# Kernel tuning notes

Measured on AMD Instinct MI355X. Metric: run time of the kernel, lower is better.

## Reference

```python
import jax, jax.numpy as jnp
import numpy as np
from jax import lax

B, L, C, H, W = 16, 8, 64, 50, 50
OC, K, PAD = 64, 3, 1
CQ = C // 16


def conv2d(x, w, b, pad):
    y = lax.conv_general_dilated(x, w, (1, 1), [(pad, pad), (pad, pad)],
                                 dimension_numbers=('NCHW', 'OIHW', 'NCHW'))
    return y + b[None, :, None, None]


def attention(x, y, q_w, q_b, k_w, k_b, v_w, v_b):
    # x, y: [b, C, 5, 5]
    b, c, h, w = x.shape
    q = conv2d(x, q_w, q_b, 1).reshape(b, -1, h * w)   # [b, CQ, N]
    kk = conv2d(y, k_w, k_b, 1).reshape(b, -1, h * w)  # [b, CQ, N]
    attn = jax.nn.softmax(jnp.einsum('bcn,bcm->bnm', q, kk), axis=-1)  # [b, Nq, Nk]
    v = conv2d(y, v_w, v_b, 1).reshape(b, c, h * w)    # [b, C, N]
    out = jnp.einsum('bcm,bnm->bcn', v, attn)          # bmm(V, attn^T)
    return out.reshape(b, c, h, w)


def setup_inputs():
    key = jax.random.key(0)
    ks = jax.random.split(key, 15)
    s = 0.05
    return {
        'x': jax.random.normal(ks[0], (B, L, C, H, W), jnp.float32),
        'weight': jax.random.normal(ks[1], (OC, C, K, K), jnp.float32) * s,
        'bias': jax.random.normal(ks[2], (OC,), jnp.float32) * s,
        'init_w': jax.random.normal(ks[3], (C, C, 3, 3), jnp.float32) * s,
        'init_b': jax.random.normal(ks[4], (C,), jnp.float32) * s,
        'q_w': jax.random.normal(ks[5], (CQ, C, 3, 3), jnp.float32) * s,
        'q_b': jax.random.normal(ks[6], (CQ,), jnp.float32) * s,
        'k_w': jax.random.normal(ks[7], (CQ, C, 3, 3), jnp.float32) * s,
        'k_b': jax.random.normal(ks[8], (CQ,), jnp.float32) * s,
        'v_w': jax.random.normal(ks[9], (C, C, 3, 3), jnp.float32) * s,
        'v_b': jax.random.normal(ks[10], (C,), jnp.float32) * s,
        'tconv_w': jax.random.normal(ks[11], (C, C), jnp.float32) * s,  # 1x1x1 Conv3d C->C
        'tconv_b': jax.random.normal(ks[12], (C,), jnp.float32) * s,
        'fc_w': jax.random.normal(ks[13], (C,), jnp.float32) * s,       # 1x1x1 Conv3d C->1
        'fc_b': jax.random.normal(ks[14], (), jnp.float32) * s,
    }


def reference(x, weight, bias, init_w, init_b, q_w, q_b, k_w, k_b, v_w, v_b,
              tconv_w, tconv_b, fc_w, fc_b):
    b, l, c, h, w = x.shape
    # --- generateweight ---
    xet = jnp.transpose(x, (0, 2, 1, 3, 4))  # [b, c, l, h, w]
    # AdaptiveMaxPool3d((None,5,5)); h,w multiples of 5 -> exact reshape max
    pooled = xet.reshape(b, c, l, 5, h // 5, 5, w // 5).max((4, 6))  # [b,c,l,5,5]
    seq = jnp.moveaxis(pooled, 2, 0)  # [l, b, c, 5, 5]
    prior0 = conv2d(seq[0], init_w, init_b, 1)

    def step(prior, xt):
        new = attention(prior, xt, q_w, q_b, k_w, k_b, v_w, v_b)
        return new, new

    _, allp = lax.scan(step, prior0, seq)            # [l, b, c, 5, 5]
    avg = jnp.moveaxis(allp, 0, 2).mean((3, 4))      # AdaptiveAvgPool3d -> [b, c, l]
    calib = jnp.einsum('oc,bcl->bol', tconv_w, avg) + tconv_b[None, :, None]  # [b,c,l]
    scale = 1.0 + jnp.transpose(calib, (0, 2, 1))    # [b, l, c]
    # finalweight[b,l,o,i,kh,kw] = weight[o,i,kh,kw] * scale[b,l,i]
    fw = weight[None, None] * scale[:, :, None, :, None, None]
    fc_out = jnp.einsum('c,bcl->bl', fc_w, avg) + fc_b  # [b, l]
    fb = bias[None, None, :] * (1.0 + fc_out)[:, :, None]  # [b, l, oc]
    # --- grouped conv with groups = b*l ---
    xg = x.reshape(1, b * l * c, h, w)
    wg = fw.reshape(b * l * OC, c, K, K)
    out = lax.conv_general_dilated(xg, wg, (1, 1), [(PAD, PAD), (PAD, PAD)],
                                   feature_group_count=b * l,
                                   dimension_numbers=('NCHW', 'OIHW', 'NCHW'))
    out = out.reshape(b * l, OC, out.shape[-2], out.shape[-1])
    out = out + fb.reshape(b * l, OC)[:, :, None, None]
    return out
```

## Files before the change

kernel.cpp:

```cpp
#include <hip/hip_runtime.h>

typedef short s16x8 __attribute__((ext_vector_type(8)));
typedef float f32x4 __attribute__((ext_vector_type(4)));
typedef unsigned int u32x4 __attribute__((ext_vector_type(4)));

__device__ __forceinline__ unsigned short bf16r(float f) {
  unsigned int u = __float_as_uint(f);
  u += 0x7fffu + ((u >> 16) & 1u);
  return (unsigned short)(u >> 16);
}
__device__ __forceinline__ float bf_lo(unsigned int u) {
  return __uint_as_float(u << 16);
}
__device__ __forceinline__ float bf_hi(unsigned int u) {
  return __uint_as_float(u & 0xffff0000u);
}


__global__ __launch_bounds__(256) void poolprep2_kernel(
    const float* __restrict__ x, float* __restrict__ pooled,
    unsigned short* __restrict__ xs) {
  const int blk = blockIdx.x;
  const int g = blk / 10;
  const int rem = blk % 10;
  const int band = rem >> 1;
  const int chalf = rem & 1;
  const int ch0 = chalf * 4;
  const float* xg = x + (size_t)g * 160000;
  unsigned short* xsg = xs + (size_t)g * (52 * 52 * 64);
  __shared__ float pm2[32 * 250];
  const int tid = threadIdx.x;

  for (int task = tid; task < 1000; task += 256) {
    int chunk4 = task & 3;
    int rest = task >> 2;
    int xpair = rest % 25;
    int r = rest / 25;
    int y = band * 10 + r;
    int chunk = ch0 + chunk4;
    const float* base = xg + (chunk * 8) * 2500 + y * 50 + xpair * 2;
    float2 v[8];
#pragma unroll
    for (int k = 0; k < 8; ++k) v[k] = *(const float2*)(base + k * 2500);
#pragma unroll
    for (int k = 0; k < 8; ++k)
      pm2[(chunk4 * 8 + k) * 250 + r * 25 + xpair] = fmaxf(v[k].x, v[k].y);
    uint4 a, b;
    a.x = (unsigned)bf16r(v[0].x) | ((unsigned)bf16r(v[1].x) << 16);
    a.y = (unsigned)bf16r(v[2].x) | ((unsigned)bf16r(v[3].x) << 16);
    a.z = (unsigned)bf16r(v[4].x) | ((unsigned)bf16r(v[5].x) << 16);
    a.w = (unsigned)bf16r(v[6].x) | ((unsigned)bf16r(v[7].x) << 16);
    b.x = (unsigned)bf16r(v[0].y) | ((unsigned)bf16r(v[1].y) << 16);
    b.y = (unsigned)bf16r(v[2].y) | ((unsigned)bf16r(v[3].y) << 16);
    b.z = (unsigned)bf16r(v[4].y) | ((unsigned)bf16r(v[5].y) << 16);
    b.w = (unsigned)bf16r(v[6].y) | ((unsigned)bf16r(v[7].y) << 16);
    int xx = xpair * 2;
    *(uint4*)&xsg[(((y + 1) * 52) + (xx + 1)) * 64 + chunk * 8] = a;
    *(uint4*)&xsg[(((y + 1) * 52) + (xx + 2)) * 64 + chunk * 8] = b;
  }
  uint4 z4;
  z4.x = 0; z4.y = 0; z4.z = 0; z4.w = 0;
  for (int task = tid; task < 80; task += 256) {
    int chunk4 = task & 3;
    int rest = task >> 2;
    int col = (rest & 1) ? 51 : 0;
    int r = rest >> 1;
    int y = band * 10 + r;
    *(uint4*)&xsg[(((y + 1) * 52) + col) * 64 + (ch0 + chunk4) * 8] = z4;
  }
  if (band == 0) {
    for (int task = tid; task < 208; task += 256)
      *(uint4*)&xsg[(task >> 2) * 64 + (ch0 + (task & 3)) * 8] = z4;
  }
  if (band == 4) {
    for (int task = tid; task < 208; task += 256)
      *(uint4*)&xsg[(51 * 52 + (task >> 2)) * 64 + (ch0 + (task & 3)) * 8] = z4;
  }
  __syncthreads();
  if (tid < 160) {
    int c_local = tid / 5, ox = tid % 5;
    const float* pr = &pm2[c_local * 250 + ox * 5];
    float m = -1e30f;
#pragma unroll
    for (int r = 0; r < 10; ++r) {
#pragma unroll
      for (int xp = 0; xp < 5; ++xp) m = fmaxf(m, pr[r * 25 + xp]);
    }
    int c_g = chalf * 32 + c_local;
    pooled[(size_t)g * 1600 + c_g * 25 + band * 5 + ox] = m;
  }
}

__device__ __forceinline__ void conv_pass2(
    const unsigned short* in_s, const unsigned short* __restrict__ wg,
    f32x4 acc[4][4], int ikk, int wave, int lane, int l15, int l4) {
#pragma unroll
  for (int dy = 0; dy < 3; ++dy) {
    const int rr = wave + dy;
#pragma unroll
    for (int dx = 0; dx < 3; ++dx) {
      const int tap = dy * 3 + dx;
      s16x8 a[4], bfr[4];
#pragma unroll
      for (int mf = 0; mf < 4; ++mf)
        a[mf] = *reinterpret_cast<const s16x8*>(
            wg + ((((tap * 2 + ikk) * 4 + mf) * 64 + lane) << 3));
#pragma unroll
      for (int nf = 0; nf < 4; ++nf) {
        int cc = nf * 16 + l15 + dx;
        int slot = l4 ^ ((cc >> 1) & 3);
        bfr[nf] = *reinterpret_cast<const s16x8*>(
            &in_s[((rr * 66 + cc) << 5) + (slot << 3)]);
      }
#pragma unroll
      for (int mf = 0; mf < 4; ++mf)
#pragma unroll
        for (int nf = 0; nf < 4; ++nf)
          acc[mf][nf] = __builtin_amdgcn_mfma_f32_16x16x32_bf16(
              a[mf], bfr[nf], acc[mf][nf], 0, 0, 0);
    }
  }
}

__global__ __launch_bounds__(512, 4) void conv_main_fast4(
    const unsigned short* __restrict__ xs, const unsigned short* __restrict__ wt3,
    const float* __restrict__ fb_g, float* __restrict__ out) {
  const int g = blockIdx.x & 127;
  const int band = blockIdx.x >> 7;
  const int y0 = band * 8;
  const int tid = threadIdx.x;
  __shared__ __align__(16) unsigned short in_s[10 * 66 * 32];
  __shared__ float fb_s[64];
  if (tid < 64) fb_s[tid] = fb_g[g * 64 + tid];

  const unsigned short* xsg = xs + (size_t)g * (52 * 52 * 64);
  const unsigned short* wg = wt3 + (size_t)g * 36864;
  const int wave = tid >> 6, lane = tid & 63;
  const int l15 = lane & 15, l4 = lane >> 4;
  const int yrow = y0 + wave;

  f32x4 acc[4][4];
  f32x4 z = {0.f, 0.f, 0.f, 0.f};
#pragma unroll
  for (int mf = 0; mf < 4; ++mf)
#pragma unroll
    for (int nf = 0; nf < 4; ++nf) acc[mf][nf] = z;

  for (int task = tid; task < 2640; task += 512) {
    int slot = task & 3;
    int c = (task >> 2) % 66;
    int r = (task >> 2) / 66;
    int py = y0 + r;
    int srcSub = slot ^ ((c >> 1) & 3);
    const unsigned short* src = xsg + ((size_t)(py * 52 + c) * 64 + srcSub * 8);
    unsigned short* ldsb = in_s + (size_t)(task & ~63) * 8;
    __builtin_amdgcn_global_load_lds(
        (const __attribute__((address_space(1))) void*)src,
        (__attribute__((address_space(3))) void*)ldsb, 16, 0, 0);
  }
  __syncthreads();
  if (yrow < 50) conv_pass2(in_s, wg, acc, 0, wave, lane, l15, l4);
  __syncthreads();
  for (int task = tid; task < 2640; task += 512) {
    int slot = task & 3;
    int c = (task >> 2) % 66;
    int r = (task >> 2) / 66;
    int py = y0 + r;
    int srcSub = slot ^ ((c >> 1) & 3);
    const unsigned short* src = xsg + ((size_t)(py * 52 + c) * 64 + 32 + srcSub * 8);
    unsigned short* ldsb = in_s + (size_t)(task & ~63) * 8;
    __builtin_amdgcn_global_load_lds(
        (const __attribute__((address_space(1))) void*)src,
        (__attribute__((address_space(3))) void*)ldsb, 16, 0, 0);
  }
  __syncthreads();
  if (yrow < 50) {
    conv_pass2(in_s, wg, acc, 1, wave, lane, l15, l4);
    float* og = out + (size_t)g * 64 * 2500 + yrow * 50;
#pragma unroll
    for (int mf = 0; mf < 4; ++mf) {
#pragma unroll
      for (int r = 0; r < 4; ++r) {
        int o = mf * 16 + l4 * 4 + r;
        float fbv = fb_s[o];
#pragma unroll
        for (int nf = 0; nf < 4; ++nf) {
          int xx = nf * 16 + l15;
          if (xx < 50) og[(size_t)o * 2500 + xx] = acc[mf][nf][r] + fbv;
        }
      }
    }
  }
}

__global__ __launch_bounds__(256) void calwt_kernel(
    const float* __restrict__ avgg, const float* __restrict__ tconvw,
    const float* __restrict__ tconvb, const float* __restrict__ fcw,
    const float* __restrict__ fcb, const float* __restrict__ bias,
    const float* __restrict__ w, float* __restrict__ fb_g,
    unsigned short* __restrict__ wt3) {
  const int g = blockIdx.x;
  const int tid = threadIdx.x;
  __shared__ float tcw_s[64 * 65];
  __shared__ float av[64];
  __shared__ float sc[64];
  for (int idx = tid; idx < 4096; idx += 256)
    tcw_s[(idx >> 6) * 65 + (idx & 63)] = tconvw[idx];
  if (tid < 64) av[tid] = avgg[g * 64 + tid];
  __syncthreads();
  if (tid < 64) {
    int o = tid;
    float cal = tconvb[o];
#pragma unroll
    for (int c = 0; c < 64; ++c) cal += tcw_s[o * 65 + c] * av[c];
    sc[o] = 1.0f + cal;
    float part = fcw[o] * av[o];
#pragma unroll
    for (int off = 32; off; off >>= 1) part += __shfl_down(part, off);
    float fc = __shfl(part, 0) + fcb[0];
    fb_g[g * 64 + o] = bias[o] * (1.0f + fc);
  }
  __syncthreads();
  unsigned short* outg = wt3 + (size_t)g * 36864;
  for (int idx = tid; idx < 36864; idx += 256) {
    int j = idx & 7;
    int lane = (idx >> 3) & 63;
    int mf = (idx >> 9) & 3;
    int ik = (idx >> 11) & 1;
    int tap = idx >> 12;
    int o = mf * 16 + (lane & 15);
    int i = ik * 32 + 8 * (lane >> 4) + j;
    outg[idx] = bf16r(w[((o * 64) + i) * 9 + tap] * sc[i]);
  }
}


__device__ __forceinline__ void conv64core(const float* pool_s,
                                           const float* __restrict__ wgt,
                                           float* red, int tid) {
  int co = tid & 63, qd = tid >> 6;
  float acc[25];
#pragma unroll
  for (int n = 0; n < 25; ++n) acc[n] = 0.f;
  for (int ci = qd * 16; ci < qd * 16 + 16; ++ci) {
    float in[25];
#pragma unroll
    for (int n = 0; n < 25; ++n) in[n] = pool_s[ci * 25 + n];
    float w9[9];
#pragma unroll
    for (int tp = 0; tp < 9; ++tp) w9[tp] = wgt[(co * 64 + ci) * 9 + tp];
#pragma unroll
    for (int n = 0; n < 25; ++n) {
      int y = n / 5, xx = n % 5;
#pragma unroll
      for (int dy = 0; dy < 3; ++dy) {
        int yy = y + dy - 1;
        if (yy < 0 || yy > 4) continue;
#pragma unroll
        for (int dx = 0; dx < 3; ++dx) {
          int xc = xx + dx - 1;
          if (xc < 0 || xc > 4) continue;
          acc[n] += in[yy * 5 + xc] * w9[dy * 3 + dx];
        }
      }
    }
  }
#pragma unroll
  for (int n = 0; n < 25; ++n) red[(qd * 64 + co) * 25 + n] = acc[n];
  __syncthreads();
}

__global__ __launch_bounds__(256) void convB2_kernel(
    const float* __restrict__ pooled, const float* __restrict__ vw,
    const float* __restrict__ vb, const float* __restrict__ kw,
    const float* __restrict__ kb, const float* __restrict__ iw,
    const float* __restrict__ ib, unsigned short* __restrict__ vbg,
    float* __restrict__ kk4g, float* __restrict__ p28g) {
  const int blk = blockIdx.x;
  __shared__ float pool_s[1600];
  __shared__ float red[6400];
  const int tid = threadIdx.x;
  for (int idx = tid; idx < 1600; idx += 256) pool_s[idx] = pooled[blk * 1600 + idx];
  __syncthreads();

  conv64core(pool_s, vw, red, tid);
  {
    unsigned short* dst = vbg + (size_t)blk * 2560;
    for (int idx = tid; idx < 1600; idx += 256) {
      float s = red[idx] + red[1600 + idx] + red[3200 + idx] + red[4800 + idx];
      dst[(idx / 25) * 40 + idx % 25] = bf16r(s + vb[idx / 25]);
    }
    for (int idx = tid; idx < 960; idx += 256)
      dst[(idx / 15) * 40 + 25 + idx % 15] = 0;
  }
  __syncthreads();

  {
    int co = tid & 3, ci = tid >> 2;
    float acc[25];
#pragma unroll
    for (int n = 0; n < 25; ++n) acc[n] = 0.f;
    float in[25];
#pragma unroll
    for (int n = 0; n < 25; ++n) in[n] = pool_s[ci * 25 + n];
    float w9[9];
#pragma unroll
    for (int tp = 0; tp < 9; ++tp) w9[tp] = kw[(co * 64 + ci) * 9 + tp];
#pragma unroll
    for (int n = 0; n < 25; ++n) {
      int y = n / 5, xx = n % 5;
#pragma unroll
      for (int dy = 0; dy < 3; ++dy) {
        int yy = y + dy - 1;
        if (yy < 0 || yy > 4) continue;
#pragma unroll
        for (int dx = 0; dx < 3; ++dx) {
          int xc = xx + dx - 1;
          if (xc < 0 || xc > 4) continue;
          acc[n] += in[yy * 5 + xc] * w9[dy * 3 + dx];
        }
      }
    }
#pragma unroll
    for (int n = 0; n < 25; ++n) red[(ci * 4 + co) * 25 + n] = acc[n];
  }
  __syncthreads();
  if (tid < 100) {
    int co = tid / 25, m = tid % 25;
    float s = 0.f;
    for (int c = 0; c < 64; ++c) s += red[(c * 4 + co) * 25 + m];
    kk4g[blk * 100 + m * 4 + co] = s + kb[co];
  }
  __syncthreads();

  if ((blk & 7) == 0) {
    conv64core(pool_s, iw, red, tid);
    float* dst = p28g + (size_t)(blk >> 3) * 1792;
    for (int idx = tid; idx < 1600; idx += 256) {
      float s = red[idx] + red[1600 + idx] + red[3200 + idx] + red[4800 + idx];
      dst[(idx / 25) * 28 + idx % 25] = s + ib[idx / 25];
    }
  }
}


__global__ __launch_bounds__(256) void scan3_kernel(
    const unsigned short* __restrict__ vbg, const float* __restrict__ kk4g,
    const float* __restrict__ p28g, const float* __restrict__ qw,
    const float* __restrict__ qb, float* __restrict__ avgg) {
  const int b = blockIdx.x;
  const int tid = threadIdx.x;
  __shared__ __align__(16) unsigned short v_bf[8 * 64 * 40];
  __shared__ __align__(16) unsigned short attn_bf[25 * 32];
  __shared__ float p_s[64 * 28];
  __shared__ float red[100 * 68];
  __shared__ f32x4 kk4_s[8 * 25];
  __shared__ float q_s[100];
  __shared__ float qw_s[2304];
  __shared__ float avgp[256];
  __shared__ float qb_s[4];

  {
    const u32x4* vs = (const u32x4*)(vbg + (size_t)b * 20480);
    u32x4* vd = (u32x4*)v_bf;
    for (int i = tid; i < 2560; i += 256) vd[i] = vs[i];
    const f32x4* ks = (const f32x4*)(kk4g + b * 800);
    for (int i = tid; i < 200; i += 256) kk4_s[i] = ks[i];
    const f32x4* ps = (const f32x4*)(p28g + (size_t)b * 1792);
    f32x4* pd = (f32x4*)p_s;
    for (int i = tid; i < 448; i += 256) pd[i] = ps[i];
    const f32x4* qs = (const f32x4*)qw;
    f32x4* qd = (f32x4*)qw_s;
    for (int i = tid; i < 576; i += 256) qd[i] = qs[i];
    if (tid < 4) qb_s[tid] = qb[tid];
  }
  __syncthreads();

  const int qco = tid & 3, qci = tid >> 2;
  float qwr[9];
#pragma unroll
  for (int tp = 0; tp < 9; ++tp) qwr[tp] = qw_s[(qco * 64 + qci) * 9 + tp];

#pragma unroll 1
  for (int l = 0; l < 8; ++l) {
    {
      f32x4 i4[7];
      const f32x4* pr = (const f32x4*)&p_s[qci * 28];
#pragma unroll
      for (int j = 0; j < 7; ++j) i4[j] = pr[j];
      float in[25];
#pragma unroll
      for (int n = 0; n < 25; ++n) in[n] = i4[n >> 2][n & 3];
      float acc[25];
#pragma unroll
      for (int n = 0; n < 25; ++n) acc[n] = 0.f;
#pragma unroll
      for (int n = 0; n < 25; ++n) {
        int y = n / 5, xx = n % 5;
#pragma unroll
        for (int dy = 0; dy < 3; ++dy) {
          int yy = y + dy - 1;
          if (yy < 0 || yy > 4) continue;
#pragma unroll
          for (int dx = 0; dx < 3; ++dx) {
            int xc = xx + dx - 1;
            if (xc < 0 || xc > 4) continue;
            acc[n] += in[yy * 5 + xc] * qwr[dy * 3 + dx];
          }
        }
      }
#pragma unroll
      for (int n = 0; n < 25; ++n) red[(qco * 25 + n) * 68 + qci] = acc[n];
    }
    if (l > 0 && tid < 64) {
      f32x4 a4 = *(const f32x4*)&avgp[tid * 4];
      avgg[(b * 8 + l - 1) * 64 + tid] = (a4[0] + a4[1] + a4[2] + a4[3]) * 0.04f;
    }
    __syncthreads();

    if (tid < 200) {
      int row = tid >> 1, h = tid & 1;
      const f32x4* rp = (const f32x4*)&red[row * 68 + h * 32];
      float s = 0.f;
#pragma unroll
      for (int j = 0; j < 8; ++j) {
        f32x4 r4 = rp[j];
        s += r4[0] + r4[1] + r4[2] + r4[3];
      }
      s += __shfl_down(s, 1);
      if (h == 0) q_s[row] = s + qb_s[row / 25];
    }
    __syncthreads();

    if (tid < 25) {
      const int n = tid;
      const f32x4* kk = &kk4_s[l * 25];
      float q0 = q_s[n], q1 = q_s[25 + n], q2 = q_s[50 + n], q3 = q_s[75 + n];
      float row[25];
      float mx = -1e30f;
#pragma unroll
      for (int m = 0; m < 25; ++m) {
        f32x4 k4 = kk[m];
        float s = q0 * k4[0] + q1 * k4[1] + q2 * k4[2] + q3 * k4[3];
        row[m] = s;
        mx = fmaxf(mx, s);
      }
      float sm = 0.f;
#pragma unroll
      for (int m = 0; m < 25; ++m) {
        float e = __expf(row[m] - mx);
        row[m] = e;
        sm += e;
      }
      float inv = 1.0f / sm;
      unsigned int w16[16];
#pragma unroll
      for (int j = 0; j < 16; ++j) {
        float lo = (2 * j < 25) ? row[2 * j] * inv : 0.f;
        float hi = (2 * j + 1 < 25) ? row[2 * j + 1] * inv : 0.f;
        w16[j] = (unsigned)bf16r(lo) | ((unsigned)bf16r(hi) << 16);
      }
      u32x4* ad = (u32x4*)&attn_bf[n * 32];
      u32x4 d0 = {w16[0], w16[1], w16[2], w16[3]};
      u32x4 d1 = {w16[4], w16[5], w16[6], w16[7]};
      u32x4 d2 = {w16[8], w16[9], w16[10], w16[11]};
      u32x4 d3 = {w16[12], w16[13], w16[14], w16[15]};
      ad[0] = d0; ad[1] = d1; ad[2] = d2; ad[3] = d3;
    }
    __syncthreads();

    {
      const int c = tid & 63, grp = tid >> 6;
      const u32x4* vr = (const u32x4*)&v_bf[(l * 64 + c) * 40];
      u32x4 vv[4];
#pragma unroll
      for (int j = 0; j < 4; ++j) vv[j] = vr[j];
      float vf[25];
#pragma unroll
      for (int m = 0; m < 25; ++m) {
        unsigned int u = vv[m >> 3][(m >> 1) & 3];
        vf[m] = (m & 1) ? bf_hi(u) : bf_lo(u);
      }
      float partial = 0.f;
      for (int n = grp; n < 25; n += 4) {
        const u32x4* ar = (const u32x4*)&attn_bf[n * 32];
        u32x4 aa[4];
#pragma unroll
        for (int j = 0; j < 4; ++j) aa[j] = ar[j];
        float acc = 0.f;
#pragma unroll
        for (int m = 0; m < 25; ++m) {
          unsigned int u = aa[m >> 3][(m >> 1) & 3];
          float a = (m & 1) ? bf_hi(u) : bf_lo(u);
          acc += vf[m] * a;
        }
        p_s[c * 28 + n] = acc;
        partial += acc;
      }
      avgp[(c << 2) + grp] = partial;
    }
    __syncthreads();
  }
  if (tid < 64) {
    f32x4 a4 = *(const f32x4*)&avgp[tid * 4];
    avgg[(b * 8 + 7) * 64 + tid] = (a4[0] + a4[1] + a4[2] + a4[3]) * 0.04f;
  }
}


__global__ __launch_bounds__(256) void pool_kernel(const float* __restrict__ x,
                                                   float* __restrict__ pooled) {
  const int blk = blockIdx.x;
  const float* plane = x + (size_t)blk * 2500;
  __shared__ float pmax[250];
  const int t = threadIdx.x;
  if (t < 250) {
    int r = t / 5, cc = t % 5;
    const float* row = plane + r * 50 + cc * 10;
    float m = row[0];
#pragma unroll
    for (int j = 1; j < 10; ++j) m = fmaxf(m, row[j]);
    pmax[r * 5 + cc] = m;
  }
  __syncthreads();
  if (t < 25) {
    int pr = t / 5, cc = t % 5;
    float m = pmax[(pr * 10) * 5 + cc];
#pragma unroll
    for (int rr = 1; rr < 10; ++rr) m = fmaxf(m, pmax[(pr * 10 + rr) * 5 + cc]);
    pooled[(size_t)blk * 25 + t] = m;
  }
}

__global__ __launch_bounds__(256) void wt_kernel(const float* __restrict__ w,
                                                 unsigned short* __restrict__ wt2) {
  int idx = blockIdx.x * 256 + threadIdx.x;
  if (idx >= 36864) return;
  int j = idx & 7;
  int lane = (idx >> 3) & 63;
  int mf = (idx >> 9) & 3;
  int ik = (idx >> 11) & 1;
  int tap = idx >> 12;
  int o = mf * 16 + (lane & 15);
  int i = ik * 32 + 8 * (lane >> 4) + j;
  wt2[idx] = bf16r(w[((o * 64) + i) * 9 + tap]);
}

__global__ __launch_bounds__(256) void conv_main(
    const float* __restrict__ x, const unsigned short* __restrict__ wt2,
    const float* __restrict__ scale_g, const float* __restrict__ fb_g,
    float* __restrict__ out) {
  const int g = blockIdx.x & 127;
  const int band = blockIdx.x >> 7;
  const int y0 = band * 4;
  const int tid = threadIdx.x;
  __shared__ unsigned short in_s[6 * 66 * 64];
  __shared__ float scale_s[64], fb_s[64];
  if (tid < 64) {
    scale_s[tid] = scale_g[g * 64 + tid];
    fb_s[tid] = fb_g[g * 64 + tid];
  }
  __syncthreads();
  const float* xg = x + (size_t)g * 160000;
  for (int task = tid; task < 3168; task += 256) {
    int c = task % 66;
    int rc = task / 66;
    int r = rc >> 3;
    int chunk = rc & 7;
    int y = y0 - 1 + r;
    int xi = c - 1;
    unsigned int p0 = 0, p1 = 0, p2 = 0, p3 = 0;
    if (y >= 0 && y < 50 && xi >= 0 && xi < 50) {
      const float* px = xg + chunk * 8 * 2500 + y * 50 + xi;
      float f0 = px[0] * scale_s[chunk * 8 + 0];
      float f1 = px[2500] * scale_s[chunk * 8 + 1];
      float f2 = px[5000] * scale_s[chunk * 8 + 2];
      float f3 = px[7500] * scale_s[chunk * 8 + 3];
      float f4 = px[10000] * scale_s[chunk * 8 + 4];
      float f5 = px[12500] * scale_s[chunk * 8 + 5];
      float f6 = px[15000] * scale_s[chunk * 8 + 6];
      float f7 = px[17500] * scale_s[chunk * 8 + 7];
      p0 = (unsigned)bf16r(f0) | ((unsigned)bf16r(f1) << 16);
      p1 = (unsigned)bf16r(f2) | ((unsigned)bf16r(f3) << 16);
      p2 = (unsigned)bf16r(f4) | ((unsigned)bf16r(f5) << 16);
      p3 = (unsigned)bf16r(f6) | ((unsigned)bf16r(f7) << 16);
    }
    int chS = chunk ^ (c & 7);
    uint4* dst = (uint4*)&in_s[((r * 66 + c) << 6) + (chS << 3)];
    uint4 u4;
    u4.x = p0; u4.y = p1; u4.z = p2; u4.w = p3;
    *dst = u4;
  }
  __syncthreads();
  const int wave = tid >> 6, lane = tid & 63;
  const int l15 = lane & 15, l4 = lane >> 4;
  const int yrow = y0 + wave;
  if (yrow < 50) {
    f32x4 acc[4][4];
    f32x4 z = {0.f, 0.f, 0.f, 0.f};
#pragma unroll
    for (int mf = 0; mf < 4; ++mf)
#pragma unroll
      for (int nf = 0; nf < 4; ++nf) acc[mf][nf] = z;
#pragma unroll
    for (int dy = 0; dy < 3; ++dy) {
      const int rr = wave + dy;
#pragma unroll
      for (int dx = 0; dx < 3; ++dx) {
        const int tap = dy * 3 + dx;
#pragma unroll
        for (int ik = 0; ik < 2; ++ik) {
          s16x8 a[4], bfr[4];
#pragma unroll
          for (int mf = 0; mf < 4; ++mf)
            a[mf] = *reinterpret_cast<const s16x8*>(
                wt2 + ((((tap * 2 + ik) * 4 + mf) * 64 + lane) << 3));
#pragma unroll
          for (int nf = 0; nf < 4; ++nf) {
            int cc = nf * 16 + l15 + dx;
            int chS = (ik * 4 + l4) ^ (cc & 7);
            bfr[nf] = *reinterpret_cast<const s16x8*>(
                &in_s[((rr * 66 + cc) << 6) + (chS << 3)]);
          }
#pragma unroll
          for (int mf = 0; mf < 4; ++mf)
#pragma unroll
            for (int nf = 0; nf < 4; ++nf)
              acc[mf][nf] = __builtin_amdgcn_mfma_f32_16x16x32_bf16(
                  a[mf], bfr[nf], acc[mf][nf], 0, 0, 0);
        }
      }
    }
    float* og = out + (size_t)g * 64 * 2500 + yrow * 50;
#pragma unroll
    for (int mf = 0; mf < 4; ++mf) {
#pragma unroll
      for (int r = 0; r < 4; ++r) {
        int o = mf * 16 + l4 * 4 + r;
        float fbv = fb_s[o];
#pragma unroll
        for (int nf = 0; nf < 4; ++nf) {
          int xx = nf * 16 + l15;
          if (xx < 50) og[(size_t)o * 2500 + xx] = acc[mf][nf][r] + fbv;
        }
      }
    }
  }
}

__global__ __launch_bounds__(256) void calib_kernel(
    const float* __restrict__ avgg, const float* __restrict__ tconvw,
    const float* __restrict__ tconvb, const float* __restrict__ fcw,
    const float* __restrict__ fcb, const float* __restrict__ bias,
    float* __restrict__ scale_g, float* __restrict__ fb_g) {
  const int tid = threadIdx.x;
  const int wave = tid >> 6, o = tid & 63;
  const int bl = blockIdx.x * 4 + wave;
  __shared__ float tcw_s[64 * 65];
  __shared__ float avgl[4][64];
  for (int idx = tid; idx < 4096; idx += 256)
    tcw_s[(idx >> 6) * 65 + (idx & 63)] = tconvw[idx];
  avgl[wave][o] = avgg[bl * 64 + o];
  __syncthreads();
  float cal = tconvb[o];
  const float* av = avgl[wave];
#pragma unroll
  for (int c = 0; c < 64; ++c) cal += tcw_s[o * 65 + c] * av[c];
  scale_g[bl * 64 + o] = 1.0f + cal;
  float part = fcw[o] * av[o];
#pragma unroll
  for (int off = 32; off; off >>= 1) part += __shfl_down(part, off);
  float fc = __shfl(part, 0) + fcb[0];
  fb_g[bl * 64 + o] = bias[o] * (1.0f + fc);
}

extern "C" void kernel_launch(void* const* d_in, const int* in_sizes, int n_in,
                              void* d_out, int out_size, void* d_ws, size_t ws_size,
                              hipStream_t stream) {
  const float* x       = (const float*)d_in[0];
  const float* weight  = (const float*)d_in[1];
  const float* bias    = (const float*)d_in[2];
  const float* init_w  = (const float*)d_in[3];
  const float* init_b  = (const float*)d_in[4];
  const float* q_w     = (const float*)d_in[5];
  const float* q_b     = (const float*)d_in[6];
  const float* k_w     = (const float*)d_in[7];
  const float* k_b     = (const float*)d_in[8];
  const float* v_w     = (const float*)d_in[9];
  const float* v_b     = (const float*)d_in[10];
  const float* tconv_w = (const float*)d_in[11];
  const float* tconv_b = (const float*)d_in[12];
  const float* fc_w    = (const float*)d_in[13];
  const float* fc_b    = (const float*)d_in[14];
  float* out = (float*)d_out;

  float* ws = (float*)d_ws;
  float* pooled = ws;
  unsigned short* vbg = (unsigned short*)(ws + 204800);
  float* kk4g   = ws + 368640;
  float* p28g   = ws + 381440;
  float* scaleg = ws + 410112;
  float* fbg    = ws + 418304;
  float* avgg   = ws + 426496;
  unsigned short* wt3 = (unsigned short*)(ws + 434688);
  unsigned short* xsb = wt3 + 4718592;

  const size_t NEED_FAST = 55543808ull;

  if (ws_size >= NEED_FAST) {
    poolprep2_kernel<<<1280, 256, 0, stream>>>(x, pooled, xsb);
    convB2_kernel<<<128, 256, 0, stream>>>(pooled, v_w, v_b, k_w, k_b, init_w,
                                           init_b, vbg, kk4g, p28g);
    scan3_kernel<<<16, 256, 0, stream>>>(vbg, kk4g, p28g, q_w, q_b, avgg);
    calwt_kernel<<<128, 256, 0, stream>>>(avgg, tconv_w, tconv_b, fc_w, fc_b, bias,
                                          weight, fbg, wt3);
    conv_main_fast4<<<896, 512, 0, stream>>>(xsb, wt3, fbg, out);
  } else {
    unsigned short* wt2 = (unsigned short*)(ws + 434688);
    pool_kernel<<<8192, 256, 0, stream>>>(x, pooled);
    wt_kernel<<<144, 256, 0, stream>>>(weight, wt2);
    convB2_kernel<<<128, 256, 0, stream>>>(pooled, v_w, v_b, k_w, k_b, init_w,
                                           init_b, vbg, kk4g, p28g);
    scan3_kernel<<<16, 256, 0, stream>>>(vbg, kk4g, p28g, q_w, q_b, avgg);
    calib_kernel<<<32, 256, 0, stream>>>(avgg, tconv_w, tconv_b, fc_w, fc_b, bias,
                                         scaleg, fbg);
    conv_main<<<13 * 128, 256, 0, stream>>>(x, wt2, scaleg, fbg, out);
  }
}
```

Measured before the change: 151.5 us.

## Overlap bf16 input repacking with serial scan and double-buffer conv channel halves

Splits the pooling+repack kernel so the padded bf16 input repack runs as extra blocks inside the 16-block serial attention scan kernel. The repack then fills otherwise idle CUs while the scan runs, and the pool kernel gets lighter. The main conv now uses 6-row bands with 384 threads and separate LDS buffers for the two channel halves. This lets the second half's global-to-LDS load be issued before the first half's MFMA pass, removing one barrier. The cost is more blocks, more halo row reloads from the smaller bands, larger LDS per block, and dynamic shared memory for the scan kernel.

```diff
diff --git a/kernel.cpp b/kernel.cpp
--- a/kernel.cpp
+++ b/kernel.cpp
@@ -17,9 +17,8 @@
 }
 
 
-__global__ __launch_bounds__(256) void poolprep2_kernel(
-    const float* __restrict__ x, float* __restrict__ pooled,
-    unsigned short* __restrict__ xs) {
+__global__ __launch_bounds__(256) void pool3_kernel(
+    const float* __restrict__ x, float* __restrict__ pooled) {
   const int blk = blockIdx.x;
   const int g = blk / 10;
   const int rem = blk % 10;
@@ -27,7 +26,6 @@
   const int chalf = rem & 1;
   const int ch0 = chalf * 4;
   const float* xg = x + (size_t)g * 160000;
-  unsigned short* xsg = xs + (size_t)g * (52 * 52 * 64);
   __shared__ float pm2[32 * 250];
   const int tid = threadIdx.x;
 
@@ -45,6 +43,44 @@
 #pragma unroll
     for (int k = 0; k < 8; ++k)
       pm2[(chunk4 * 8 + k) * 250 + r * 25 + xpair] = fmaxf(v[k].x, v[k].y);
+  }
+  __syncthreads();
+  if (tid < 160) {
+    int c_local = tid / 5, ox = tid % 5;
+    const float* pr = &pm2[c_local * 250 + ox * 5];
+    float m = -1e30f;
+#pragma unroll
+    for (int r = 0; r < 10; ++r) {
+#pragma unroll
+      for (int xp = 0; xp < 5; ++xp) m = fmaxf(m, pr[r * 25 + xp]);
+    }
+    int c_g = chalf * 32 + c_local;
+    pooled[(size_t)g * 1600 + c_g * 25 + band * 5 + ox] = m;
+  }
+}
+
+__device__ __forceinline__ void xsprep_block(int blk, const float* __restrict__ x,
+                                             unsigned short* __restrict__ xs) {
+  const int g = blk / 10;
+  const int rem = blk % 10;
+  const int band = rem >> 1;
+  const int chalf = rem & 1;
+  const int ch0 = chalf * 4;
+  const float* xg = x + (size_t)g * 160000;
+  unsigned short* xsg = xs + (size_t)g * (52 * 52 * 64);
+  const int tid = threadIdx.x;
+
+  for (int task = tid; task < 1000; task += 256) {
+    int chunk4 = task & 3;
+    int rest = task >> 2;
+    int xpair = rest % 25;
+    int r = rest / 25;
+    int y = band * 10 + r;
+    int chunk = ch0 + chunk4;
+    const float* base = xg + (chunk * 8) * 2500 + y * 50 + xpair * 2;
+    float2 v[8];
+#pragma unroll
+    for (int k = 0; k < 8; ++k) v[k] = *(const float2*)(base + k * 2500);
     uint4 a, b;
     a.x = (unsigned)bf16r(v[0].x) | ((unsigned)bf16r(v[1].x) << 16);
     a.y = (unsigned)bf16r(v[2].x) | ((unsigned)bf16r(v[3].x) << 16);
@@ -76,18 +112,175 @@
     for (int task = tid; task < 208; task += 256)
       *(uint4*)&xsg[(51 * 52 + (task >> 2)) * 64 + (ch0 + (task & 3)) * 8] = z4;
   }
-  __syncthreads();
-  if (tid < 160) {
-    int c_local = tid / 5, ox = tid % 5;
-    const float* pr = &pm2[c_local * 250 + ox * 5];
-    float m = -1e30f;
-#pragma unroll
-    for (int r = 0; r < 10; ++r) {
-#pragma unroll
-      for (int xp = 0; xp < 5; ++xp) m = fmaxf(m, pr[r * 25 + xp]);
-    }
-    int c_g = chalf * 32 + c_local;
-    pooled[(size_t)g * 1600 + c_g * 25 + band * 5 + ox] = m;
+}
+
+__global__ __launch_bounds__(256) void scanx_kernel(
+    const unsigned short* __restrict__ vbg, const float* __restrict__ kk4g,
+    const float* __restrict__ p28g, const float* __restrict__ qw,
+    const float* __restrict__ qb, float* __restrict__ avgg,
+    const float* __restrict__ x, unsigned short* __restrict__ xs) {
+  if (blockIdx.x >= 16) {
+    xsprep_block(blockIdx.x - 16, x, xs);
+    return;
+  }
+  extern __shared__ __align__(16) char smem_raw[];
+  unsigned short* v_bf = (unsigned short*)smem_raw;
+  unsigned short* attn_bf = (unsigned short*)(smem_raw + 40960);
+  float* p_s = (float*)(smem_raw + 42560);
+  float* red = (float*)(smem_raw + 49728);
+  f32x4* kk4_s = (f32x4*)(smem_raw + 76928);
+  float* q_s = (float*)(smem_raw + 80128);
+  float* qw_s = (float*)(smem_raw + 80528);
+  float* avgp = (float*)(smem_raw + 89744);
+  float* qb_s = (float*)(smem_raw + 90768);
+
+  const int b = blockIdx.x;
+  const int tid = threadIdx.x;
+
+  {
+    const u32x4* vs = (const u32x4*)(vbg + (size_t)b * 20480);
+    u32x4* vd = (u32x4*)v_bf;
+    for (int i = tid; i < 2560; i += 256) vd[i] = vs[i];
+    const f32x4* ks = (const f32x4*)(kk4g + b * 800);
+    for (int i = tid; i < 200; i += 256) kk4_s[i] = ks[i];
+    const f32x4* ps = (const f32x4*)(p28g + (size_t)b * 1792);
+    f32x4* pd = (f32x4*)p_s;
+    for (int i = tid; i < 448; i += 256) pd[i] = ps[i];
+    const f32x4* qs = (const f32x4*)qw;
+    f32x4* qd = (f32x4*)qw_s;
+    for (int i = tid; i < 576; i += 256) qd[i] = qs[i];
+    if (tid < 4) qb_s[tid] = qb[tid];
+  }
+  __syncthreads();
+
+  const int qco = tid & 3, qci = tid >> 2;
+  float qwr[9];
+#pragma unroll
+  for (int tp = 0; tp < 9; ++tp) qwr[tp] = qw_s[(qco * 64 + qci) * 9 + tp];
+
+#pragma unroll 1
+  for (int l = 0; l < 8; ++l) {
+    {
+      f32x4 i4[7];
+      const f32x4* pr = (const f32x4*)&p_s[qci * 28];
+#pragma unroll
+      for (int j = 0; j < 7; ++j) i4[j] = pr[j];
+      float in[25];
+#pragma unroll
+      for (int n = 0; n < 25; ++n) in[n] = i4[n >> 2][n & 3];
+      float acc[25];
+#pragma unroll
+      for (int n = 0; n < 25; ++n) acc[n] = 0.f;
+#pragma unroll
+      for (int n = 0; n < 25; ++n) {
+        int y = n / 5, xx = n % 5;
+#pragma unroll
+        for (int dy = 0; dy < 3; ++dy) {
+          int yy = y + dy - 1;
+          if (yy < 0 || yy > 4) continue;
+#pragma unroll
+          for (int dx = 0; dx < 3; ++dx) {
+            int xc = xx + dx - 1;
+            if (xc < 0 || xc > 4) continue;
+            acc[n] += in[yy * 5 + xc] * qwr[dy * 3 + dx];
+          }
+        }
+      }
+#pragma unroll
+      for (int n = 0; n < 25; ++n) red[(qco * 25 + n) * 68 + qci] = acc[n];
+    }
+    if (l > 0 && tid < 64) {
+      f32x4 a4 = *(const f32x4*)&avgp[tid * 4];
+      avgg[(b * 8 + l - 1) * 64 + tid] = (a4[0] + a4[1] + a4[2] + a4[3]) * 0.04f;
+    }
+    __syncthreads();
+
+    if (tid < 200) {
+      int row = tid >> 1, h = tid & 1;
+      const f32x4* rp = (const f32x4*)&red[row * 68 + h * 32];
+      float s = 0.f;
+#pragma unroll
+      for (int j = 0; j < 8; ++j) {
+        f32x4 r4 = rp[j];
+        s += r4[0] + r4[1] + r4[2] + r4[3];
+      }
+      s += __shfl_down(s, 1);
+      if (h == 0) q_s[row] = s + qb_s[row / 25];
+    }
+    __syncthreads();
+
+    if (tid < 25) {
+      const int n = tid;
+      const f32x4* kk = &kk4_s[l * 25];
+      float q0 = q_s[n], q1 = q_s[25 + n], q2 = q_s[50 + n], q3 = q_s[75 + n];
+      float row[25];
+      float mx = -1e30f;
+#pragma unroll
+      for (int m = 0; m < 25; ++m) {
+        f32x4 k4 = kk[m];
+        float s = q0 * k4[0] + q1 * k4[1] + q2 * k4[2] + q3 * k4[3];
+        row[m] = s;
+        mx = fmaxf(mx, s);
+      }
+      float sm = 0.f;
+#pragma unroll
+      for (int m = 0; m < 25; ++m) {
+        float e = __expf(row[m] - mx);
+        row[m] = e;
+        sm += e;
+      }
+      float inv = 1.0f / sm;
+      unsigned int w16[16];
+#pragma unroll
+      for (int j = 0; j < 16; ++j) {
+        float lo = (2 * j < 25) ? row[2 * j] * inv : 0.f;
+        float hi = (2 * j + 1 < 25) ? row[2 * j + 1] * inv : 0.f;
+        w16[j] = (unsigned)bf16r(lo) | ((unsigned)bf16r(hi) << 16);
+      }
+      u32x4* ad = (u32x4*)&attn_bf[n * 32];
+      u32x4 d0 = {w16[0], w16[1], w16[2], w16[3]};
+      u32x4 d1 = {w16[4], w16[5], w16[6], w16[7]};
+      u32x4 d2 = {w16[8], w16[9], w16[10], w16[11]};
+      u32x4 d3 = {w16[12], w16[13], w16[14], w16[15]};
+      ad[0] = d0; ad[1] = d1; ad[2] = d2; ad[3] = d3;
+    }
+    __syncthreads();
+
+    {
+      const int c = tid & 63, grp = tid >> 6;
+      const u32x4* vr = (const u32x4*)&v_bf[(l * 64 + c) * 40];
+      u32x4 vv[4];
+#pragma unroll
+      for (int j = 0; j < 4; ++j) vv[j] = vr[j];
+      float vf[25];
+#pragma unroll
+      for (int m = 0; m < 25; ++m) {
+        unsigned int u = vv[m >> 3][(m >> 1) & 3];
+        vf[m] = (m & 1) ? bf_hi(u) : bf_lo(u);
+      }
+      float partial = 0.f;
+      for (int n = grp; n < 25; n += 4) {
+        const u32x4* ar = (const u32x4*)&attn_bf[n * 32];
+        u32x4 aa[4];
+#pragma unroll
+        for (int j = 0; j < 4; ++j) aa[j] = ar[j];
+        float acc = 0.f;
+#pragma unroll
+        for (int m = 0; m < 25; ++m) {
+          unsigned int u = aa[m >> 3][(m >> 1) & 3];
+          float a = (m & 1) ? bf_hi(u) : bf_lo(u);
+          acc += vf[m] * a;
+        }
+        p_s[c * 28 + n] = acc;
+        partial += acc;
+      }
+      avgp[(c << 2) + grp] = partial;
+    }
+    __syncthreads();
+  }
+  if (tid < 64) {
+    f32x4 a4 = *(const f32x4*)&avgp[tid * 4];
+    avgg[(b * 8 + 7) * 64 + tid] = (a4[0] + a4[1] + a4[2] + a4[3]) * 0.04f;
   }
 }
 
@@ -122,14 +315,15 @@
   }
 }
 
-__global__ __launch_bounds__(512, 4) void conv_main_fast4(
+__global__ __launch_bounds__(384, 3) void conv_main_fast5(
     const unsigned short* __restrict__ xs, const unsigned short* __restrict__ wt3,
     const float* __restrict__ fb_g, float* __restrict__ out) {
   const int g = blockIdx.x & 127;
   const int band = blockIdx.x >> 7;
-  const int y0 = band * 8;
+  const int y0 = band * 6;
   const int tid = threadIdx.x;
-  __shared__ __align__(16) unsigned short in_s[10 * 66 * 32];
+  __shared__ __align__(16) unsigned short in0[8 * 66 * 32];
+  __shared__ __align__(16) unsigned short in1[8 * 66 * 32];
   __shared__ float fb_s[64];
   if (tid < 64) fb_s[tid] = fb_g[g * 64 + tid];
 
@@ -146,36 +340,35 @@
 #pragma unroll
     for (int nf = 0; nf < 4; ++nf) acc[mf][nf] = z;
 
-  for (int task = tid; task < 2640; task += 512) {
+  for (int task = tid; task < 2112; task += 384) {
     int slot = task & 3;
     int c = (task >> 2) % 66;
     int r = (task >> 2) / 66;
     int py = y0 + r;
     int srcSub = slot ^ ((c >> 1) & 3);
     const unsigned short* src = xsg + ((size_t)(py * 52 + c) * 64 + srcSub * 8);
-    unsigned short* ldsb = in_s + (size_t)(task & ~63) * 8;
+    unsigned short* ldsb = in0 + (size_t)(task & ~63) * 8;
     __builtin_amdgcn_global_load_lds(
         (const __attribute__((address_space(1))) void*)src,
         (__attribute__((address_space(3))) void*)ldsb, 16, 0, 0);
   }
   __syncthreads();
-  if (yrow < 50) conv_pass2(in_s, wg, acc, 0, wave, lane, l15, l4);
-  __syncthreads();
-  for (int task = tid; task < 2640; task += 512) {
+  for (int task = tid; task < 2112; task += 384) {
     int slot = task & 3;
     int c = (task >> 2) % 66;
     int r = (task >> 2) / 66;
     int py = y0 + r;
     int srcSub = slot ^ ((c >> 1) & 3);
     const unsigned short* src = xsg + ((size_t)(py * 52 + c) * 64 + 32 + srcSub * 8);
-    unsigned short* ldsb = in_s + (size_t)(task & ~63) * 8;
+    unsigned short* ldsb = in1 + (size_t)(task & ~63) * 8;
     __builtin_amdgcn_global_load_lds(
         (const __attribute__((address_space(1))) void*)src,
         (__attribute__((address_space(3))) void*)ldsb, 16, 0, 0);
   }
+  if (yrow < 50) conv_pass2(in0, wg, acc, 0, wave, lane, l15, l4);
   __syncthreads();
   if (yrow < 50) {
-    conv_pass2(in_s, wg, acc, 1, wave, lane, l15, l4);
+    conv_pass2(in1, wg, acc, 1, wave, lane, l15, l4);
     float* og = out + (size_t)g * 64 * 2500 + yrow * 50;
 #pragma unroll
     for (int mf = 0; mf < 4; ++mf) {
@@ -340,170 +533,6 @@
       float s = red[idx] + red[1600 + idx] + red[3200 + idx] + red[4800 + idx];
       dst[(idx / 25) * 28 + idx % 25] = s + ib[idx / 25];
     }
-  }
-}
-
-
-__global__ __launch_bounds__(256) void scan3_kernel(
-    const unsigned short* __restrict__ vbg, const float* __restrict__ kk4g,
-    const float* __restrict__ p28g, const float* __restrict__ qw,
-    const float* __restrict__ qb, float* __restrict__ avgg) {
-  const int b = blockIdx.x;
-  const int tid = threadIdx.x;
-  __shared__ __align__(16) unsigned short v_bf[8 * 64 * 40];
-  __shared__ __align__(16) unsigned short attn_bf[25 * 32];
-  __shared__ float p_s[64 * 28];
-  __shared__ float red[100 * 68];
-  __shared__ f32x4 kk4_s[8 * 25];
-  __shared__ float q_s[100];
-  __shared__ float qw_s[2304];
-  __shared__ float avgp[256];
-  __shared__ float qb_s[4];
-
-  {
-    const u32x4* vs = (const u32x4*)(vbg + (size_t)b * 20480);
-    u32x4* vd = (u32x4*)v_bf;
-    for (int i = tid; i < 2560; i += 256) vd[i] = vs[i];
-    const f32x4* ks = (const f32x4*)(kk4g + b * 800);
-    for (int i = tid; i < 200; i += 256) kk4_s[i] = ks[i];
-    const f32x4* ps = (const f32x4*)(p28g + (size_t)b * 1792);
-    f32x4* pd = (f32x4*)p_s;
-    for (int i = tid; i < 448; i += 256) pd[i] = ps[i];
-    const f32x4* qs = (const f32x4*)qw;
-    f32x4* qd = (f32x4*)qw_s;
-    for (int i = tid; i < 576; i += 256) qd[i] = qs[i];
-    if (tid < 4) qb_s[tid] = qb[tid];
-  }
-  __syncthreads();
-
-  const int qco = tid & 3, qci = tid >> 2;
-  float qwr[9];
-#pragma unroll
-  for (int tp = 0; tp < 9; ++tp) qwr[tp] = qw_s[(qco * 64 + qci) * 9 + tp];
-
-#pragma unroll 1
-  for (int l = 0; l < 8; ++l) {
-    {
-      f32x4 i4[7];
-      const f32x4* pr = (const f32x4*)&p_s[qci * 28];
-#pragma unroll
-      for (int j = 0; j < 7; ++j) i4[j] = pr[j];
-      float in[25];
-#pragma unroll
-      for (int n = 0; n < 25; ++n) in[n] = i4[n >> 2][n & 3];
-      float acc[25];
-#pragma unroll
-      for (int n = 0; n < 25; ++n) acc[n] = 0.f;
-#pragma unroll
-      for (int n = 0; n < 25; ++n) {
-        int y = n / 5, xx = n % 5;
-#pragma unroll
-        for (int dy = 0; dy < 3; ++dy) {
-          int yy = y + dy - 1;
-          if (yy < 0 || yy > 4) continue;
-#pragma unroll
-          for (int dx = 0; dx < 3; ++dx) {
-            int xc = xx + dx - 1;
-            if (xc < 0 || xc > 4) continue;
-            acc[n] += in[yy * 5 + xc] * qwr[dy * 3 + dx];
-          }
-        }
-      }
-#pragma unroll
-      for (int n = 0; n < 25; ++n) red[(qco * 25 + n) * 68 + qci] = acc[n];
-    }
-    if (l > 0 && tid < 64) {
-      f32x4 a4 = *(const f32x4*)&avgp[tid * 4];
-      avgg[(b * 8 + l - 1) * 64 + tid] = (a4[0] + a4[1] + a4[2] + a4[3]) * 0.04f;
-    }
-    __syncthreads();
-
-    if (tid < 200) {
-      int row = tid >> 1, h = tid & 1;
-      const f32x4* rp = (const f32x4*)&red[row * 68 + h * 32];
-      float s = 0.f;
-#pragma unroll
-      for (int j = 0; j < 8; ++j) {
-        f32x4 r4 = rp[j];
-        s += r4[0] + r4[1] + r4[2] + r4[3];
-      }
-      s += __shfl_down(s, 1);
-      if (h == 0) q_s[row] = s + qb_s[row / 25];
-    }
-    __syncthreads();
-
-    if (tid < 25) {
-      const int n = tid;
-      const f32x4* kk = &kk4_s[l * 25];
-      float q0 = q_s[n], q1 = q_s[25 + n], q2 = q_s[50 + n], q3 = q_s[75 + n];
-      float row[25];
-      float mx = -1e30f;
-#pragma unroll
-      for (int m = 0; m < 25; ++m) {
-        f32x4 k4 = kk[m];
-        float s = q0 * k4[0] + q1 * k4[1] + q2 * k4[2] + q3 * k4[3];
-        row[m] = s;
-        mx = fmaxf(mx, s);
-      }
-      float sm = 0.f;
-#pragma unroll
-      for (int m = 0; m < 25; ++m) {
-        float e = __expf(row[m] - mx);
-        row[m] = e;
-        sm += e;
-      }
-      float inv = 1.0f / sm;
-      unsigned int w16[16];
-#pragma unroll
-      for (int j = 0; j < 16; ++j) {
-        float lo = (2 * j < 25) ? row[2 * j] * inv : 0.f;
-        float hi = (2 * j + 1 < 25) ? row[2 * j + 1] * inv : 0.f;
-        w16[j] = (unsigned)bf16r(lo) | ((unsigned)bf16r(hi) << 16);
-      }
-      u32x4* ad = (u32x4*)&attn_bf[n * 32];
-      u32x4 d0 = {w16[0], w16[1], w16[2], w16[3]};
-      u32x4 d1 = {w16[4], w16[5], w16[6], w16[7]};
-      u32x4 d2 = {w16[8], w16[9], w16[10], w16[11]};
-      u32x4 d3 = {w16[12], w16[13], w16[14], w16[15]};
-      ad[0] = d0; ad[1] = d1; ad[2] = d2; ad[3] = d3;
-    }
-    __syncthreads();
-
-    {
-      const int c = tid & 63, grp = tid >> 6;
-      const u32x4* vr = (const u32x4*)&v_bf[(l * 64 + c) * 40];
-      u32x4 vv[4];
-#pragma unroll
-      for (int j = 0; j < 4; ++j) vv[j] = vr[j];
-      float vf[25];
-#pragma unroll
-      for (int m = 0; m < 25; ++m) {
-        unsigned int u = vv[m >> 3][(m >> 1) & 3];
-        vf[m] = (m & 1) ? bf_hi(u) : bf_lo(u);
-      }
-      float partial = 0.f;
-      for (int n = grp; n < 25; n += 4) {
-        const u32x4* ar = (const u32x4*)&attn_bf[n * 32];
-        u32x4 aa[4];
-#pragma unroll
-        for (int j = 0; j < 4; ++j) aa[j] = ar[j];
-        float acc = 0.f;
-#pragma unroll
-        for (int m = 0; m < 25; ++m) {
-          unsigned int u = aa[m >> 3][(m >> 1) & 3];
-          float a = (m & 1) ? bf_hi(u) : bf_lo(u);
-          acc += vf[m] * a;
-        }
-        p_s[c * 28 + n] = acc;
-        partial += acc;
-      }
-      avgp[(c << 2) + grp] = partial;
-    }
-    __syncthreads();
-  }
-  if (tid < 64) {
-    f32x4 a4 = *(const f32x4*)&avgp[tid * 4];
-    avgg[(b * 8 + 7) * 64 + tid] = (a4[0] + a4[1] + a4[2] + a4[3]) * 0.04f;
   }
 }
 
@@ -706,22 +735,25 @@
   unsigned short* xsb = wt3 + 4718592;
 
   const size_t NEED_FAST = 55543808ull;
+  const unsigned SCAN_LDS = 90784;
 
   if (ws_size >= NEED_FAST) {
-    poolprep2_kernel<<<1280, 256, 0, stream>>>(x, pooled, xsb);
+    pool3_kernel<<<1280, 256, 0, stream>>>(x, pooled);
     convB2_kernel<<<128, 256, 0, stream>>>(pooled, v_w, v_b, k_w, k_b, init_w,
                                            init_b, vbg, kk4g, p28g);
-    scan3_kernel<<<16, 256, 0, stream>>>(vbg, kk4g, p28g, q_w, q_b, avgg);
+    scanx_kernel<<<16 + 1280, 256, SCAN_LDS, stream>>>(vbg, kk4g, p28g, q_w, q_b,
+                                                       avgg, x, xsb);
     calwt_kernel<<<128, 256, 0, stream>>>(avgg, tconv_w, tconv_b, fc_w, fc_b, bias,
                                           weight, fbg, wt3);
-    conv_main_fast4<<<896, 512, 0, stream>>>(xsb, wt3, fbg, out);
+    conv_main_fast5<<<9 * 128, 384, 0, stream>>>(xsb, wt3, fbg, out);
   } else {
     unsigned short* wt2 = (unsigned short*)(ws + 434688);
     pool_kernel<<<8192, 256, 0, stream>>>(x, pooled);
     wt_kernel<<<144, 256, 0, stream>>>(weight, wt2);
     convB2_kernel<<<128, 256, 0, stream>>>(pooled, v_w, v_b, k_w, k_b, init_w,
                                            init_b, vbg, kk4g, p28g);
-    scan3_kernel<<<16, 256, 0, stream>>>(vbg, kk4g, p28g, q_w, q_b, avgg);
+    scanx_kernel<<<16, 256, SCAN_LDS, stream>>>(vbg, kk4g, p28g, q_w, q_b,
+                                                avgg, x, (unsigned short*)0);
     calib_kernel<<<32, 256, 0, stream>>>(avgg, tconv_w, tconv_b, fc_w, fc_b, bias,
                                          scaleg, fbg);
     conv_main<<<13 * 128, 256, 0, stream>>>(x, wt2, scaleg, fbg, out);
```

After: 168.1 us. +10.9%, slower.
